# Kernel tuning notes

Hardware: AMD Instinct MI355X
Metric: run time of the kernel (lower is better)

## Reference

```python
import jax, jax.numpy as jnp
import numpy as np

D_MODEL = 2048
N_HEADS = 16
HEAD_DIM = 128
KV_RANK = 512


def setup_inputs() -> dict:
    key = jax.random.key(0)
    ks = jax.random.split(key, 6)
    s = lambda fan_in: 1.0 / np.sqrt(fan_in)
    return {
        "x": jax.random.normal(ks[0], (2, 2048, D_MODEL), dtype=jnp.float32),
        "Wq": jax.random.normal(ks[1], (D_MODEL, N_HEADS * HEAD_DIM), dtype=jnp.float32) * s(D_MODEL),
        "Wdown": jax.random.normal(ks[2], (D_MODEL, KV_RANK), dtype=jnp.float32) * s(D_MODEL),
        "Wk_up": jax.random.normal(ks[3], (KV_RANK, N_HEADS * HEAD_DIM), dtype=jnp.float32) * s(KV_RANK),
        "Wv_up": jax.random.normal(ks[4], (KV_RANK, N_HEADS * HEAD_DIM), dtype=jnp.float32) * s(KV_RANK),
        "Wo": jax.random.normal(ks[5], (N_HEADS * HEAD_DIM, D_MODEL), dtype=jnp.float32) * s(N_HEADS * HEAD_DIM),
    }


def reference(x, Wq, Wdown, Wk_up, Wv_up, Wo):
    B, T, _ = x.shape
    H, Dh = N_HEADS, HEAD_DIM
    # Q projection: (B,T,H,Dh) -> (B,H,T,Dh)
    Q = (x @ Wq).reshape(B, T, H, Dh).transpose(0, 2, 1, 3)
    # latent compression (this is the cached tensor)
    c = x @ Wdown  # (B, T, kv_lora_rank)
    # up-project latent to full K/V heads
    K = (c @ Wk_up).reshape(B, T, H, Dh).transpose(0, 2, 1, 3)
    V = (c @ Wv_up).reshape(B, T, H, Dh).transpose(0, 2, 1, 3)
    # causal SDPA (mask=None, past_kv=None -> is_causal=True), dropout=0
    scale = Dh ** (-0.5)
    scores = jnp.einsum("bhqd,bhkd->bhqk", Q, K) * scale
    causal = jnp.tril(jnp.ones((T, T), dtype=bool))
    scores = jnp.where(causal[None, None], scores, jnp.finfo(scores.dtype).min)
    attn = jax.nn.softmax(scores, axis=-1)
    out = jnp.einsum("bhqk,bhkd->bhqd", attn, V)
    out = out.transpose(0, 2, 1, 3).reshape(B, T, H * Dh)
    return out @ Wo, c
```

## Files before the change

### kernel.cpp

```cpp
#include <hip/hip_runtime.h>

typedef short bf16x8 __attribute__((ext_vector_type(8)));
typedef float f32x4 __attribute__((ext_vector_type(4)));

__device__ __forceinline__ void async16(const void* g, const void* l) {
  __builtin_amdgcn_global_load_lds(
      (const __attribute__((address_space(1))) unsigned int*)g,
      (__attribute__((address_space(3))) unsigned int*)(void*)(uintptr_t)l,
      16, 0, 0);
}

__device__ __forceinline__ unsigned short f2b(float f) {
  unsigned int u = __float_as_uint(f);
  u += 0x7fffu + ((u >> 16) & 1u);
  return (unsigned short)(u >> 16);
}

__global__ __launch_bounds__(256) void cast_f32_bf16(
    const float* __restrict__ in, unsigned short* __restrict__ out, int n) {
  int i = (blockIdx.x * 256 + threadIdx.x) * 4;
  if (i < n) {
    float4 v = *(const float4*)(in + i);
    ushort4 o;
    o.x = f2b(v.x); o.y = f2b(v.y); o.z = f2b(v.z); o.w = f2b(v.w);
    *(ushort4*)(out + i) = o;
  }
}

__global__ __launch_bounds__(256) void transpose_cast(
    const float* __restrict__ in, unsigned short* __restrict__ out,
    int K, int N) {
  __shared__ __align__(16) unsigned short tile[64][65];
  const int k0 = blockIdx.y * 64, n0 = blockIdx.x * 64;
  const int tid = threadIdx.x;
  const int r = tid >> 4, c4 = tid & 15;
#pragma unroll
  for (int p = 0; p < 4; ++p) {
    int row = p * 16 + r;
    float4 v = *(const float4*)(in + (size_t)(k0 + row) * N + n0 + c4 * 4);
    tile[c4 * 4 + 0][row] = f2b(v.x);
    tile[c4 * 4 + 1][row] = f2b(v.y);
    tile[c4 * 4 + 2][row] = f2b(v.z);
    tile[c4 * 4 + 3][row] = f2b(v.w);
  }
  __syncthreads();
#pragma unroll
  for (int p = 0; p < 4; ++p) {
    int nr = p * 16 + r;
    ushort4 o;
    o.x = tile[nr][c4 * 4 + 0];
    o.y = tile[nr][c4 * 4 + 1];
    o.z = tile[nr][c4 * 4 + 2];
    o.w = tile[nr][c4 * 4 + 3];
    *(ushort4*)(out + (size_t)(n0 + nr) * K + k0 + c4 * 4) = o;
  }
}

__global__ __launch_bounds__(256) void transpose_bf16(
    const unsigned short* __restrict__ in, unsigned short* __restrict__ out,
    int K, int N) {
  __shared__ __align__(16) unsigned short tile[64][65];
  const int k0 = blockIdx.y * 64, n0 = blockIdx.x * 64;
  const int tid = threadIdx.x;
  const int r = tid >> 4, c4 = tid & 15;
#pragma unroll
  for (int p = 0; p < 4; ++p) {
    int row = p * 16 + r;
    ushort4 v = *(const ushort4*)(in + (size_t)(k0 + row) * N + n0 + c4 * 4);
    tile[c4 * 4 + 0][row] = v.x;
    tile[c4 * 4 + 1][row] = v.y;
    tile[c4 * 4 + 2][row] = v.z;
    tile[c4 * 4 + 3][row] = v.w;
  }
  __syncthreads();
#pragma unroll
  for (int p = 0; p < 4; ++p) {
    int nr = p * 16 + r;
    ushort4 o;
    o.x = tile[nr][c4 * 4 + 0];
    o.y = tile[nr][c4 * 4 + 1];
    o.z = tile[nr][c4 * 4 + 2];
    o.w = tile[nr][c4 * 4 + 3];
    *(ushort4*)(out + (size_t)(n0 + nr) * K + k0 + c4 * 4) = o;
  }
}

__global__ __launch_bounds__(256) void gemm_bt(
    const unsigned short* __restrict__ A, const unsigned short* __restrict__ BT,
    unsigned short* __restrict__ Cb, float* __restrict__ Cf, int M, int N, int K) {
  __shared__ __align__(16) unsigned short sA[128 * 64];
  __shared__ __align__(16) unsigned short sB[128 * 64];
  const int tid = threadIdx.x;
  const int wave = tid >> 6, lane = tid & 63;
  const int quad = lane >> 4, cl = lane & 15;
  const int m0 = blockIdx.y * 128, n0 = blockIdx.x * 128;
  const int wm = (wave >> 1) * 64, wn = (wave & 1) * 64;
  (void)M;

  f32x4 acc[4][4] = {};

  const unsigned short* gA = A + (size_t)(m0 + wave * 32 + (lane >> 3)) * K + (lane & 7) * 8;
  const unsigned short* gB = BT + (size_t)(n0 + wave * 32 + (lane >> 3)) * K + (lane & 7) * 8;
  char* lA = (char*)sA + (wave * 32) * 128;
  char* lB = (char*)sB + (wave * 32) * 128;

  for (int kt = 0; kt < K; kt += 64) {
#pragma unroll
    for (int r = 0; r < 4; ++r) {
      async16(gA + (size_t)r * 8 * K + kt, lA + r * 8 * 128);
      async16(gB + (size_t)r * 8 * K + kt, lB + r * 8 * 128);
    }
    __syncthreads();
#pragma unroll
    for (int kk = 0; kk < 64; kk += 32) {
      bf16x8 af[4], bfr[4];
#pragma unroll
      for (int i = 0; i < 4; ++i)
        af[i] = *(const bf16x8*)((const char*)sA + (wm + i * 16 + cl) * 128 + kk * 2 + quad * 16);
#pragma unroll
      for (int j = 0; j < 4; ++j)
        bfr[j] = *(const bf16x8*)((const char*)sB + (wn + j * 16 + cl) * 128 + kk * 2 + quad * 16);
#pragma unroll
      for (int i = 0; i < 4; ++i)
#pragma unroll
        for (int j = 0; j < 4; ++j)
          acc[i][j] = __builtin_amdgcn_mfma_f32_16x16x32_bf16(af[i], bfr[j], acc[i][j], 0, 0, 0);
    }
    __syncthreads();
  }
#pragma unroll
  for (int i = 0; i < 4; ++i)
#pragma unroll
    for (int j = 0; j < 4; ++j)
#pragma unroll
      for (int r = 0; r < 4; ++r) {
        int row = m0 + wm + i * 16 + quad * 4 + r;
        int col = n0 + wn + j * 16 + cl;
        float v = acc[i][j][r];
        if (Cb) Cb[(size_t)row * N + col] = f2b(v);
        if (Cf) Cf[(size_t)row * N + col] = v;
      }
}

__global__ __launch_bounds__(256) void mla_attn(
    const unsigned short* __restrict__ Qm, const unsigned short* __restrict__ Km,
    const unsigned short* __restrict__ Vt, unsigned short* __restrict__ Om, int T) {
  const int ld = 2048;
  const int ldv = 4096;
  __shared__ __align__(16) unsigned short sK[64 * 128];
  __shared__ __align__(16) unsigned short sVT[128 * 64];
  __shared__ __align__(16) unsigned short sP[64 * 64];
  const int h = blockIdx.y, b = blockIdx.z;
  const int tid = threadIdx.x, wave = tid >> 6, lane = tid & 63;
  const int quad = lane >> 4, cl = lane & 15;
  const int nq = T / 64;
  const float scale2 = 0.08838834764831845f * 1.4426950408889634f;

  for (int phase = 0; phase < 2; ++phase) {
    const int qt = phase ? (nq - 1 - blockIdx.x) : blockIdx.x;

    bf16x8 qf[4];
    {
      const unsigned short* Qg =
          Qm + (size_t)(b * T + qt * 64 + wave * 16 + cl) * ld + h * 128 + quad * 8;
#pragma unroll
      for (int kk = 0; kk < 4; ++kk)
        qf[kk] = *(const bf16x8*)(Qg + kk * 32);
    }

    float m_i[4], l_i[4];
    f32x4 acc_o[8] = {};
#pragma unroll
    for (int r = 0; r < 4; ++r) { m_i[r] = -1e30f; l_i[r] = 0.f; }

    for (int kt = 0; kt <= qt; ++kt) {
      const unsigned short* Kg = Km + (size_t)(b * T + kt * 64) * ld + h * 128;
      const unsigned short* Vg = Vt + (size_t)(h * 128) * ldv + (size_t)b * T + kt * 64;
      __syncthreads();
#pragma unroll
      for (int r = 0; r < 4; ++r) {
        int c0 = r * 256 + wave * 64;
        int c = c0 + lane;
        int row = c >> 4, j = (c & 15) ^ (row & 7);
        async16(Kg + (size_t)row * ld + j * 8, (char*)sK + c0 * 16);
        int d = c >> 3, jv = (c & 7) ^ (d & 7);
        async16(Vg + (size_t)d * ldv + jv * 8, (char*)sVT + c0 * 16);
      }
      __syncthreads();

      f32x4 s[4] = {};
#pragma unroll
      for (int kk = 0; kk < 4; ++kk) {
#pragma unroll
        for (int j = 0; j < 4; ++j) {
          int t = j * 16 + cl;
          int jp = (kk * 4 + quad) ^ (t & 7);
          bf16x8 bk = *(const bf16x8*)((const char*)sK + (t * 16 + jp) * 16);
          s[j] = __builtin_amdgcn_mfma_f32_16x16x32_bf16(qf[kk], bk, s[j], 0, 0, 0);
        }
      }

      const bool need_mask = (kt == qt);
#pragma unroll
      for (int r = 0; r < 4; ++r) {
        int q_l = wave * 16 + quad * 4 + r;
        float mx = -1e30f;
#pragma unroll
        for (int j = 0; j < 4; ++j) {
          float v = s[j][r] * scale2;
          if (need_mask) {
            int t_l = j * 16 + cl;
            if (t_l > q_l) v = -1e30f;
          }
          s[j][r] = v;
          mx = fmaxf(mx, v);
        }
#pragma unroll
        for (int off = 1; off < 16; off <<= 1)
          mx = fmaxf(mx, __shfl_xor(mx, off));
        float m_new = fmaxf(m_i[r], mx);
        float alpha = exp2f(m_i[r] - m_new);
        m_i[r] = m_new;
        float rs = 0.f;
#pragma unroll
        for (int j = 0; j < 4; ++j) {
          float p = exp2f(s[j][r] - m_new);
          s[j][r] = p;
          rs += p;
        }
#pragma unroll
        for (int off = 1; off < 16; off <<= 1)
          rs += __shfl_xor(rs, off);
        l_i[r] = l_i[r] * alpha + rs;
#pragma unroll
        for (int jd = 0; jd < 8; ++jd)
          acc_o[jd][r] *= alpha;
      }

#pragma unroll
      for (int j = 0; j < 4; ++j)
#pragma unroll
        for (int r = 0; r < 4; ++r) {
          int q = wave * 16 + quad * 4 + r;
          int swz = (q & 7) ^ (((q >> 3) & 1) << 1);
          int t = j * 16 + cl;
          int jp = (t >> 3) ^ swz;
          sP[(q * 8 + jp) * 8 + (t & 7)] = f2b(s[j][r]);
        }

#pragma unroll
      for (int kk2 = 0; kk2 < 2; ++kk2) {
        int q = wave * 16 + cl;
        int swz = (q & 7) ^ (((q >> 3) & 1) << 1);
        int jp = (kk2 * 4 + quad) ^ swz;
        bf16x8 ap = *(const bf16x8*)((const char*)sP + (q * 8 + jp) * 16);
#pragma unroll
        for (int jd = 0; jd < 8; ++jd) {
          int d = jd * 16 + cl;
          int jpv = (kk2 * 4 + quad) ^ (d & 7);
          bf16x8 bv = *(const bf16x8*)((const char*)sVT + (d * 8 + jpv) * 16);
          acc_o[jd] = __builtin_amdgcn_mfma_f32_16x16x32_bf16(ap, bv, acc_o[jd], 0, 0, 0);
        }
      }
    }

#pragma unroll
    for (int r = 0; r < 4; ++r) {
      float inv = 1.f / l_i[r];
      int row = b * T + qt * 64 + wave * 16 + quad * 4 + r;
#pragma unroll
      for (int jd = 0; jd < 8; ++jd)
        Om[(size_t)row * ld + h * 128 + jd * 16 + cl] = f2b(acc_o[jd][r] * inv);
    }
  }
}

extern "C" void kernel_launch(void* const* d_in, const int* in_sizes, int n_in,
                              void* d_out, int out_size, void* d_ws, size_t ws_size,
                              hipStream_t stream) {
  (void)in_sizes; (void)n_in; (void)out_size; (void)ws_size;
  const int B = 2, T = 2048, Dm = 2048, H = 16, Dh = 128, R = 512;
  const int M = B * T;
  const float* x     = (const float*)d_in[0];
  const float* Wq    = (const float*)d_in[1];
  const float* Wdown = (const float*)d_in[2];
  const float* Wkup  = (const float*)d_in[3];
  const float* Wvup  = (const float*)d_in[4];
  const float* Wo    = (const float*)d_in[5];

  float* out  = (float*)d_out;
  float* cout = out + (size_t)M * Dm;

  unsigned short* ws  = (unsigned short*)d_ws;
  unsigned short* WqT = ws;
  unsigned short* WoT = WqT + (size_t)Dm * Dm;
  unsigned short* WdT = WoT + (size_t)Dm * Dm;
  unsigned short* WkT = WdT + (size_t)R * Dm;
  unsigned short* WvT = WkT + (size_t)Dm * R;
  unsigned short* xb  = WvT + (size_t)Dm * R;
  unsigned short* cb  = xb + (size_t)M * Dm;
  unsigned short* Qb  = cb + (size_t)M * R;
  unsigned short* Kb  = Qb + (size_t)M * Dm;
  unsigned short* Vb  = Kb + (size_t)M * Dm;
  unsigned short* Vtb = Vb + (size_t)M * Dm;
  unsigned short* AO  = xb;

  cast_f32_bf16<<<(M * Dm) / 1024, 256, 0, stream>>>(x, xb, M * Dm);
  transpose_cast<<<dim3(32, 32), 256, 0, stream>>>(Wq, WqT, Dm, Dm);
  transpose_cast<<<dim3(32, 32), 256, 0, stream>>>(Wo, WoT, Dm, Dm);
  transpose_cast<<<dim3(8, 32), 256, 0, stream>>>(Wdown, WdT, Dm, R);
  transpose_cast<<<dim3(32, 8), 256, 0, stream>>>(Wkup, WkT, R, Dm);
  transpose_cast<<<dim3(32, 8), 256, 0, stream>>>(Wvup, WvT, R, Dm);

  gemm_bt<<<dim3(R / 128, M / 128), 256, 0, stream>>>(xb, WdT, cb, cout, M, R, Dm);
  gemm_bt<<<dim3(Dm / 128, M / 128), 256, 0, stream>>>(xb, WqT, Qb, nullptr, M, Dm, Dm);
  gemm_bt<<<dim3(Dm / 128, M / 128), 256, 0, stream>>>(cb, WkT, Kb, nullptr, M, Dm, R);
  gemm_bt<<<dim3(Dm / 128, M / 128), 256, 0, stream>>>(cb, WvT, Vb, nullptr, M, Dm, R);

  transpose_bf16<<<dim3(Dm / 64, M / 64), 256, 0, stream>>>(Vb, Vtb, M, Dm);

  mla_attn<<<dim3(T / 128, H, B), 256, 0, stream>>>(Qb, Kb, Vtb, AO, T);

  gemm_bt<<<dim3(Dm / 128, M / 128), 256, 0, stream>>>(AO, WoT, nullptr, out, M, Dm, Dm);
  (void)Dh; (void)H;
}
```

Before: 429.4 us.

## Double-buffer K/V tiles, fold softmax scale into Q, skip small rescales

The attention kernel now double-buffers the K and V^T shared-memory tiles, so the load of the next tile is issued before computing on the current one. This removes one barrier per iteration and hides global-load latency. The softmax scale (times log2 e) is folded into the Q projection epilogue, and the running-max rescale of the output accumulator is skipped unless the max grows by more than a threshold. The trade-offs are doubled LDS use, which may lower occupancy, and a lazy rescale that lets exponentials grow up to 2^6 before renormalising.

```diff
diff --git a/kernel.cpp b/kernel.cpp
--- a/kernel.cpp
+++ b/kernel.cpp
@@ -87,7 +87,8 @@
 
 __global__ __launch_bounds__(256) void gemm_bt(
     const unsigned short* __restrict__ A, const unsigned short* __restrict__ BT,
-    unsigned short* __restrict__ Cb, float* __restrict__ Cf, int M, int N, int K) {
+    unsigned short* __restrict__ Cb, float* __restrict__ Cf, int M, int N, int K,
+    float cscale) {
   __shared__ __align__(16) unsigned short sA[128 * 64];
   __shared__ __align__(16) unsigned short sB[128 * 64];
   const int tid = threadIdx.x;
@@ -137,7 +138,7 @@
         int row = m0 + wm + i * 16 + quad * 4 + r;
         int col = n0 + wn + j * 16 + cl;
         float v = acc[i][j][r];
-        if (Cb) Cb[(size_t)row * N + col] = f2b(v);
+        if (Cb) Cb[(size_t)row * N + col] = f2b(v * cscale);
         if (Cf) Cf[(size_t)row * N + col] = v;
       }
 }
@@ -147,14 +148,13 @@
     const unsigned short* __restrict__ Vt, unsigned short* __restrict__ Om, int T) {
   const int ld = 2048;
   const int ldv = 4096;
-  __shared__ __align__(16) unsigned short sK[64 * 128];
-  __shared__ __align__(16) unsigned short sVT[128 * 64];
+  __shared__ __align__(16) unsigned short sK[2][64 * 128];
+  __shared__ __align__(16) unsigned short sVT[2][128 * 64];
   __shared__ __align__(16) unsigned short sP[64 * 64];
   const int h = blockIdx.y, b = blockIdx.z;
   const int tid = threadIdx.x, wave = tid >> 6, lane = tid & 63;
   const int quad = lane >> 4, cl = lane & 15;
   const int nq = T / 64;
-  const float scale2 = 0.08838834764831845f * 1.4426950408889634f;
 
   for (int phase = 0; phase < 2; ++phase) {
     const int qt = phase ? (nq - 1 - blockIdx.x) : blockIdx.x;
@@ -173,20 +173,40 @@
 #pragma unroll
     for (int r = 0; r < 4; ++r) { m_i[r] = -1e30f; l_i[r] = 0.f; }
 
+    const unsigned short* Kg0 = Km + (size_t)(b * T) * ld + h * 128;
+    const unsigned short* Vg0 = Vt + (size_t)(h * 128) * ldv + (size_t)b * T;
+
+#pragma unroll
+    for (int r = 0; r < 4; ++r) {
+      int c0 = r * 256 + wave * 64;
+      int c = c0 + lane;
+      int row = c >> 4, j = (c & 15) ^ (row & 7);
+      async16(Kg0 + (size_t)row * ld + j * 8, (char*)sK[0] + c0 * 16);
+      int d = c >> 3, jv = (c & 7) ^ (d & 7);
+      async16(Vg0 + (size_t)d * ldv + jv * 8, (char*)sVT[0] + c0 * 16);
+    }
+    __syncthreads();
+
     for (int kt = 0; kt <= qt; ++kt) {
-      const unsigned short* Kg = Km + (size_t)(b * T + kt * 64) * ld + h * 128;
-      const unsigned short* Vg = Vt + (size_t)(h * 128) * ldv + (size_t)b * T + kt * 64;
-      __syncthreads();
-#pragma unroll
-      for (int r = 0; r < 4; ++r) {
-        int c0 = r * 256 + wave * 64;
-        int c = c0 + lane;
-        int row = c >> 4, j = (c & 15) ^ (row & 7);
-        async16(Kg + (size_t)row * ld + j * 8, (char*)sK + c0 * 16);
-        int d = c >> 3, jv = (c & 7) ^ (d & 7);
-        async16(Vg + (size_t)d * ldv + jv * 8, (char*)sVT + c0 * 16);
-      }
-      __syncthreads();
+      const int cur = kt & 1;
+      const char* cK = (const char*)sK[cur];
+      const char* cV = (const char*)sVT[cur];
+
+      if (kt < qt) {
+        const unsigned short* Kg = Kg0 + (size_t)(kt + 1) * 64 * ld;
+        const unsigned short* Vg = Vg0 + (kt + 1) * 64;
+        char* dK = (char*)sK[cur ^ 1];
+        char* dV = (char*)sVT[cur ^ 1];
+#pragma unroll
+        for (int r = 0; r < 4; ++r) {
+          int c0 = r * 256 + wave * 64;
+          int c = c0 + lane;
+          int row = c >> 4, j = (c & 15) ^ (row & 7);
+          async16(Kg + (size_t)row * ld + j * 8, dK + c0 * 16);
+          int d = c >> 3, jv = (c & 7) ^ (d & 7);
+          async16(Vg + (size_t)d * ldv + jv * 8, dV + c0 * 16);
+        }
+      }
 
       f32x4 s[4] = {};
 #pragma unroll
@@ -195,7 +215,7 @@
         for (int j = 0; j < 4; ++j) {
           int t = j * 16 + cl;
           int jp = (kk * 4 + quad) ^ (t & 7);
-          bf16x8 bk = *(const bf16x8*)((const char*)sK + (t * 16 + jp) * 16);
+          bf16x8 bk = *(const bf16x8*)(cK + (t * 16 + jp) * 16);
           s[j] = __builtin_amdgcn_mfma_f32_16x16x32_bf16(qf[kk], bk, s[j], 0, 0, 0);
         }
       }
@@ -207,34 +227,37 @@
         float mx = -1e30f;
 #pragma unroll
         for (int j = 0; j < 4; ++j) {
-          float v = s[j][r] * scale2;
+          float v = s[j][r];
           if (need_mask) {
             int t_l = j * 16 + cl;
             if (t_l > q_l) v = -1e30f;
+            s[j][r] = v;
           }
-          s[j][r] = v;
           mx = fmaxf(mx, v);
         }
 #pragma unroll
         for (int off = 1; off < 16; off <<= 1)
           mx = fmaxf(mx, __shfl_xor(mx, off));
-        float m_new = fmaxf(m_i[r], mx);
-        float alpha = exp2f(m_i[r] - m_new);
-        m_i[r] = m_new;
+        if (__any(mx > m_i[r] + 6.f)) {
+          float m_new = fmaxf(m_i[r], mx);
+          float alpha = exp2f(m_i[r] - m_new);
+          m_i[r] = m_new;
+          l_i[r] *= alpha;
+#pragma unroll
+          for (int jd = 0; jd < 8; ++jd)
+            acc_o[jd][r] *= alpha;
+        }
         float rs = 0.f;
 #pragma unroll
         for (int j = 0; j < 4; ++j) {
-          float p = exp2f(s[j][r] - m_new);
+          float p = exp2f(s[j][r] - m_i[r]);
           s[j][r] = p;
           rs += p;
         }
 #pragma unroll
         for (int off = 1; off < 16; off <<= 1)
           rs += __shfl_xor(rs, off);
-        l_i[r] = l_i[r] * alpha + rs;
-#pragma unroll
-        for (int jd = 0; jd < 8; ++jd)
-          acc_o[jd][r] *= alpha;
+        l_i[r] += rs;
       }
 
 #pragma unroll
@@ -258,10 +281,11 @@
         for (int jd = 0; jd < 8; ++jd) {
           int d = jd * 16 + cl;
           int jpv = (kk2 * 4 + quad) ^ (d & 7);
-          bf16x8 bv = *(const bf16x8*)((const char*)sVT + (d * 8 + jpv) * 16);
+          bf16x8 bv = *(const bf16x8*)(cV + (d * 8 + jpv) * 16);
           acc_o[jd] = __builtin_amdgcn_mfma_f32_16x16x32_bf16(ap, bv, acc_o[jd], 0, 0, 0);
         }
       }
+      __syncthreads();
     }
 
 #pragma unroll
@@ -305,6 +329,8 @@
   unsigned short* Vtb = Vb + (size_t)M * Dm;
   unsigned short* AO  = xb;
 
+  const float qscale = 0.08838834764831845f * 1.4426950408889634f;
+
   cast_f32_bf16<<<(M * Dm) / 1024, 256, 0, stream>>>(x, xb, M * Dm);
   transpose_cast<<<dim3(32, 32), 256, 0, stream>>>(Wq, WqT, Dm, Dm);
   transpose_cast<<<dim3(32, 32), 256, 0, stream>>>(Wo, WoT, Dm, Dm);
@@ -312,15 +338,15 @@
   transpose_cast<<<dim3(32, 8), 256, 0, stream>>>(Wkup, WkT, R, Dm);
   transpose_cast<<<dim3(32, 8), 256, 0, stream>>>(Wvup, WvT, R, Dm);
 
-  gemm_bt<<<dim3(R / 128, M / 128), 256, 0, stream>>>(xb, WdT, cb, cout, M, R, Dm);
-  gemm_bt<<<dim3(Dm / 128, M / 128), 256, 0, stream>>>(xb, WqT, Qb, nullptr, M, Dm, Dm);
-  gemm_bt<<<dim3(Dm / 128, M / 128), 256, 0, stream>>>(cb, WkT, Kb, nullptr, M, Dm, R);
-  gemm_bt<<<dim3(Dm / 128, M / 128), 256, 0, stream>>>(cb, WvT, Vb, nullptr, M, Dm, R);
+  gemm_bt<<<dim3(R / 128, M / 128), 256, 0, stream>>>(xb, WdT, cb, cout, M, R, Dm, 1.f);
+  gemm_bt<<<dim3(Dm / 128, M / 128), 256, 0, stream>>>(xb, WqT, Qb, nullptr, M, Dm, Dm, qscale);
+  gemm_bt<<<dim3(Dm / 128, M / 128), 256, 0, stream>>>(cb, WkT, Kb, nullptr, M, Dm, R, 1.f);
+  gemm_bt<<<dim3(Dm / 128, M / 128), 256, 0, stream>>>(cb, WvT, Vb, nullptr, M, Dm, R, 1.f);
 
   transpose_bf16<<<dim3(Dm / 64, M / 64), 256, 0, stream>>>(Vb, Vtb, M, Dm);
 
   mla_attn<<<dim3(T / 128, H, B), 256, 0, stream>>>(Qb, Kb, Vtb, AO, T);
 
-  gemm_bt<<<dim3(Dm / 128, M / 128), 256, 0, stream>>>(AO, WoT, nullptr, out, M, Dm, Dm);
+  gemm_bt<<<dim3(Dm / 128, M / 128), 256, 0, stream>>>(AO, WoT, nullptr, out, M, Dm, Dm, 1.f);
   (void)Dh; (void)H;
 }
```

New measurement: 499.9 us. 1.16x slower.

## Fold softmax scale into Q projection, add lazy rescaling, one q-tile per block

Applied to the files above, without the earlier changes.

The softmax scale (including log2e) is folded into the Q GEMM epilogue, which removes a per-element multiply in attention. The online softmax now rescales the running max and accumulator only when some lane's max grows by more than a threshold of 6, skipping most alpha multiplies. The paired-q-tile loop is replaced by one q-tile per block with a doubled grid (longest tiles first), and launch bounds request 4 blocks per SM. The risks are load imbalance, since each block's work is no longer balanced by pairing, and reduced precision from rounding the scaled Q to bf16 with a lagging max.

```diff
diff --git a/kernel.cpp b/kernel.cpp
--- a/kernel.cpp
+++ b/kernel.cpp
@@ -87,7 +87,8 @@
 
 __global__ __launch_bounds__(256) void gemm_bt(
     const unsigned short* __restrict__ A, const unsigned short* __restrict__ BT,
-    unsigned short* __restrict__ Cb, float* __restrict__ Cf, int M, int N, int K) {
+    unsigned short* __restrict__ Cb, float* __restrict__ Cf, int M, int N, int K,
+    float cscale) {
   __shared__ __align__(16) unsigned short sA[128 * 64];
   __shared__ __align__(16) unsigned short sB[128 * 64];
   const int tid = threadIdx.x;
@@ -137,12 +138,12 @@
         int row = m0 + wm + i * 16 + quad * 4 + r;
         int col = n0 + wn + j * 16 + cl;
         float v = acc[i][j][r];
-        if (Cb) Cb[(size_t)row * N + col] = f2b(v);
+        if (Cb) Cb[(size_t)row * N + col] = f2b(v * cscale);
         if (Cf) Cf[(size_t)row * N + col] = v;
       }
 }
 
-__global__ __launch_bounds__(256) void mla_attn(
+__global__ __launch_bounds__(256, 4) void mla_attn(
     const unsigned short* __restrict__ Qm, const unsigned short* __restrict__ Km,
     const unsigned short* __restrict__ Vt, unsigned short* __restrict__ Om, int T) {
   const int ld = 2048;
@@ -154,124 +155,123 @@
   const int tid = threadIdx.x, wave = tid >> 6, lane = tid & 63;
   const int quad = lane >> 4, cl = lane & 15;
   const int nq = T / 64;
-  const float scale2 = 0.08838834764831845f * 1.4426950408889634f;
-
-  for (int phase = 0; phase < 2; ++phase) {
-    const int qt = phase ? (nq - 1 - blockIdx.x) : blockIdx.x;
-
-    bf16x8 qf[4];
-    {
-      const unsigned short* Qg =
-          Qm + (size_t)(b * T + qt * 64 + wave * 16 + cl) * ld + h * 128 + quad * 8;
-#pragma unroll
-      for (int kk = 0; kk < 4; ++kk)
-        qf[kk] = *(const bf16x8*)(Qg + kk * 32);
-    }
-
-    float m_i[4], l_i[4];
-    f32x4 acc_o[8] = {};
-#pragma unroll
-    for (int r = 0; r < 4; ++r) { m_i[r] = -1e30f; l_i[r] = 0.f; }
-
-    for (int kt = 0; kt <= qt; ++kt) {
-      const unsigned short* Kg = Km + (size_t)(b * T + kt * 64) * ld + h * 128;
-      const unsigned short* Vg = Vt + (size_t)(h * 128) * ldv + (size_t)b * T + kt * 64;
-      __syncthreads();
-#pragma unroll
-      for (int r = 0; r < 4; ++r) {
-        int c0 = r * 256 + wave * 64;
-        int c = c0 + lane;
-        int row = c >> 4, j = (c & 15) ^ (row & 7);
-        async16(Kg + (size_t)row * ld + j * 8, (char*)sK + c0 * 16);
-        int d = c >> 3, jv = (c & 7) ^ (d & 7);
-        async16(Vg + (size_t)d * ldv + jv * 8, (char*)sVT + c0 * 16);
-      }
-      __syncthreads();
-
-      f32x4 s[4] = {};
-#pragma unroll
-      for (int kk = 0; kk < 4; ++kk) {
-#pragma unroll
-        for (int j = 0; j < 4; ++j) {
-          int t = j * 16 + cl;
-          int jp = (kk * 4 + quad) ^ (t & 7);
-          bf16x8 bk = *(const bf16x8*)((const char*)sK + (t * 16 + jp) * 16);
-          s[j] = __builtin_amdgcn_mfma_f32_16x16x32_bf16(qf[kk], bk, s[j], 0, 0, 0);
+  const int qt = nq - 1 - blockIdx.x;
+
+  bf16x8 qf[4];
+  {
+    const unsigned short* Qg =
+        Qm + (size_t)(b * T + qt * 64 + wave * 16 + cl) * ld + h * 128 + quad * 8;
+#pragma unroll
+    for (int kk = 0; kk < 4; ++kk)
+      qf[kk] = *(const bf16x8*)(Qg + kk * 32);
+  }
+
+  float m_i[4], l_i[4];
+  f32x4 acc_o[8] = {};
+#pragma unroll
+  for (int r = 0; r < 4; ++r) { m_i[r] = -1e30f; l_i[r] = 0.f; }
+
+  for (int kt = 0; kt <= qt; ++kt) {
+    const unsigned short* Kg = Km + (size_t)(b * T + kt * 64) * ld + h * 128;
+    const unsigned short* Vg = Vt + (size_t)(h * 128) * ldv + (size_t)b * T + kt * 64;
+    __syncthreads();
+#pragma unroll
+    for (int r = 0; r < 4; ++r) {
+      int c0 = r * 256 + wave * 64;
+      int c = c0 + lane;
+      int row = c >> 4, j = (c & 15) ^ (row & 7);
+      async16(Kg + (size_t)row * ld + j * 8, (char*)sK + c0 * 16);
+      int d = c >> 3, jv = (c & 7) ^ (d & 7);
+      async16(Vg + (size_t)d * ldv + jv * 8, (char*)sVT + c0 * 16);
+    }
+    __syncthreads();
+
+    f32x4 s[4] = {};
+#pragma unroll
+    for (int kk = 0; kk < 4; ++kk) {
+#pragma unroll
+      for (int j = 0; j < 4; ++j) {
+        int t = j * 16 + cl;
+        int jp = (kk * 4 + quad) ^ (t & 7);
+        bf16x8 bk = *(const bf16x8*)((const char*)sK + (t * 16 + jp) * 16);
+        s[j] = __builtin_amdgcn_mfma_f32_16x16x32_bf16(qf[kk], bk, s[j], 0, 0, 0);
+      }
+    }
+
+    const bool need_mask = (kt == qt);
+#pragma unroll
+    for (int r = 0; r < 4; ++r) {
+      int q_l = wave * 16 + quad * 4 + r;
+      float mx = -1e30f;
+#pragma unroll
+      for (int j = 0; j < 4; ++j) {
+        float v = s[j][r];
+        if (need_mask) {
+          int t_l = j * 16 + cl;
+          if (t_l > q_l) v = -1e30f;
+          s[j][r] = v;
         }
-      }
-
-      const bool need_mask = (kt == qt);
-#pragma unroll
-      for (int r = 0; r < 4; ++r) {
-        int q_l = wave * 16 + quad * 4 + r;
-        float mx = -1e30f;
-#pragma unroll
-        for (int j = 0; j < 4; ++j) {
-          float v = s[j][r] * scale2;
-          if (need_mask) {
-            int t_l = j * 16 + cl;
-            if (t_l > q_l) v = -1e30f;
-          }
-          s[j][r] = v;
-          mx = fmaxf(mx, v);
-        }
-#pragma unroll
-        for (int off = 1; off < 16; off <<= 1)
-          mx = fmaxf(mx, __shfl_xor(mx, off));
+        mx = fmaxf(mx, v);
+      }
+#pragma unroll
+      for (int off = 1; off < 16; off <<= 1)
+        mx = fmaxf(mx, __shfl_xor(mx, off));
+      if (__any(mx > m_i[r] + 6.f)) {
         float m_new = fmaxf(m_i[r], mx);
         float alpha = exp2f(m_i[r] - m_new);
         m_i[r] = m_new;
-        float rs = 0.f;
-#pragma unroll
-        for (int j = 0; j < 4; ++j) {
-          float p = exp2f(s[j][r] - m_new);
-          s[j][r] = p;
-          rs += p;
-        }
-#pragma unroll
-        for (int off = 1; off < 16; off <<= 1)
-          rs += __shfl_xor(rs, off);
-        l_i[r] = l_i[r] * alpha + rs;
+        l_i[r] *= alpha;
 #pragma unroll
         for (int jd = 0; jd < 8; ++jd)
           acc_o[jd][r] *= alpha;
       }
-
-#pragma unroll
-      for (int j = 0; j < 4; ++j)
-#pragma unroll
-        for (int r = 0; r < 4; ++r) {
-          int q = wave * 16 + quad * 4 + r;
-          int swz = (q & 7) ^ (((q >> 3) & 1) << 1);
-          int t = j * 16 + cl;
-          int jp = (t >> 3) ^ swz;
-          sP[(q * 8 + jp) * 8 + (t & 7)] = f2b(s[j][r]);
-        }
-
-#pragma unroll
-      for (int kk2 = 0; kk2 < 2; ++kk2) {
-        int q = wave * 16 + cl;
+      float rs = 0.f;
+#pragma unroll
+      for (int j = 0; j < 4; ++j) {
+        float p = exp2f(s[j][r] - m_i[r]);
+        s[j][r] = p;
+        rs += p;
+      }
+#pragma unroll
+      for (int off = 1; off < 16; off <<= 1)
+        rs += __shfl_xor(rs, off);
+      l_i[r] += rs;
+    }
+
+#pragma unroll
+    for (int j = 0; j < 4; ++j)
+#pragma unroll
+      for (int r = 0; r < 4; ++r) {
+        int q = wave * 16 + quad * 4 + r;
         int swz = (q & 7) ^ (((q >> 3) & 1) << 1);
-        int jp = (kk2 * 4 + quad) ^ swz;
-        bf16x8 ap = *(const bf16x8*)((const char*)sP + (q * 8 + jp) * 16);
-#pragma unroll
-        for (int jd = 0; jd < 8; ++jd) {
-          int d = jd * 16 + cl;
-          int jpv = (kk2 * 4 + quad) ^ (d & 7);
-          bf16x8 bv = *(const bf16x8*)((const char*)sVT + (d * 8 + jpv) * 16);
-          acc_o[jd] = __builtin_amdgcn_mfma_f32_16x16x32_bf16(ap, bv, acc_o[jd], 0, 0, 0);
-        }
-      }
-    }
-
-#pragma unroll
-    for (int r = 0; r < 4; ++r) {
-      float inv = 1.f / l_i[r];
-      int row = b * T + qt * 64 + wave * 16 + quad * 4 + r;
-#pragma unroll
-      for (int jd = 0; jd < 8; ++jd)
-        Om[(size_t)row * ld + h * 128 + jd * 16 + cl] = f2b(acc_o[jd][r] * inv);
-    }
+        int t = j * 16 + cl;
+        int jp = (t >> 3) ^ swz;
+        sP[(q * 8 + jp) * 8 + (t & 7)] = f2b(s[j][r]);
+      }
+
+#pragma unroll
+    for (int kk2 = 0; kk2 < 2; ++kk2) {
+      int q = wave * 16 + cl;
+      int swz = (q & 7) ^ (((q >> 3) & 1) << 1);
+      int jp = (kk2 * 4 + quad) ^ swz;
+      bf16x8 ap = *(const bf16x8*)((const char*)sP + (q * 8 + jp) * 16);
+#pragma unroll
+      for (int jd = 0; jd < 8; ++jd) {
+        int d = jd * 16 + cl;
+        int jpv = (kk2 * 4 + quad) ^ (d & 7);
+        bf16x8 bv = *(const bf16x8*)((const char*)sVT + (d * 8 + jpv) * 16);
+        acc_o[jd] = __builtin_amdgcn_mfma_f32_16x16x32_bf16(ap, bv, acc_o[jd], 0, 0, 0);
+      }
+    }
+  }
+
+#pragma unroll
+  for (int r = 0; r < 4; ++r) {
+    float inv = 1.f / l_i[r];
+    int row = b * T + qt * 64 + wave * 16 + quad * 4 + r;
+#pragma unroll
+    for (int jd = 0; jd < 8; ++jd)
+      Om[(size_t)row * ld + h * 128 + jd * 16 + cl] = f2b(acc_o[jd][r] * inv);
   }
 }
 
@@ -305,6 +305,8 @@
   unsigned short* Vtb = Vb + (size_t)M * Dm;
   unsigned short* AO  = xb;
 
+  const float qscale = 0.08838834764831845f * 1.4426950408889634f;
+
   cast_f32_bf16<<<(M * Dm) / 1024, 256, 0, stream>>>(x, xb, M * Dm);
   transpose_cast<<<dim3(32, 32), 256, 0, stream>>>(Wq, WqT, Dm, Dm);
   transpose_cast<<<dim3(32, 32), 256, 0, stream>>>(Wo, WoT, Dm, Dm);
@@ -312,15 +314,15 @@
   transpose_cast<<<dim3(32, 8), 256, 0, stream>>>(Wkup, WkT, R, Dm);
   transpose_cast<<<dim3(32, 8), 256, 0, stream>>>(Wvup, WvT, R, Dm);
 
-  gemm_bt<<<dim3(R / 128, M / 128), 256, 0, stream>>>(xb, WdT, cb, cout, M, R, Dm);
-  gemm_bt<<<dim3(Dm / 128, M / 128), 256, 0, stream>>>(xb, WqT, Qb, nullptr, M, Dm, Dm);
-  gemm_bt<<<dim3(Dm / 128, M / 128), 256, 0, stream>>>(cb, WkT, Kb, nullptr, M, Dm, R);
-  gemm_bt<<<dim3(Dm / 128, M / 128), 256, 0, stream>>>(cb, WvT, Vb, nullptr, M, Dm, R);
+  gemm_bt<<<dim3(R / 128, M / 128), 256, 0, stream>>>(xb, WdT, cb, cout, M, R, Dm, 1.f);
+  gemm_bt<<<dim3(Dm / 128, M / 128), 256, 0, stream>>>(xb, WqT, Qb, nullptr, M, Dm, Dm, qscale);
+  gemm_bt<<<dim3(Dm / 128, M / 128), 256, 0, stream>>>(cb, WkT, Kb, nullptr, M, Dm, R, 1.f);
+  gemm_bt<<<dim3(Dm / 128, M / 128), 256, 0, stream>>>(cb, WvT, Vb, nullptr, M, Dm, R, 1.f);
 
   transpose_bf16<<<dim3(Dm / 64, M / 64), 256, 0, stream>>>(Vb, Vtb, M, Dm);
 
-  mla_attn<<<dim3(T / 128, H, B), 256, 0, stream>>>(Qb, Kb, Vtb, AO, T);
-
-  gemm_bt<<<dim3(Dm / 128, M / 128), 256, 0, stream>>>(AO, WoT, nullptr, out, M, Dm, Dm);
+  mla_attn<<<dim3(T / 64, H, B), 256, 0, stream>>>(Qb, Kb, Vtb, AO, T);
+
+  gemm_bt<<<dim3(Dm / 128, M / 128), 256, 0, stream>>>(AO, WoT, nullptr, out, M, Dm, Dm, 1.f);
   (void)Dh; (void)H;
 }
```

Result: slower. 515.3 us (+20.0%).
